# Optimization experiments

Hardware: AMD Instinct MI355X
Metric: run time of the kernel (lower is better)

## Reference

```python
import jax, jax.numpy as jnp
import numpy as np

KERNEL = 4  # conv kernel_size == stride


def setup_inputs() -> dict:
    key = jax.random.key(0)
    k1, k2, k3, k4 = jax.random.split(key, 4)
    x = jax.random.normal(k1, (16, 3, 512, 512), dtype=jnp.float32)
    w_sample = jax.random.normal(k2, (64, 3, KERNEL, KERNEL), dtype=jnp.float32) * 0.1
    b_sample = jax.random.normal(k3, (64,), dtype=jnp.float32) * 0.1
    centers = jax.random.uniform(k4, (8,), dtype=jnp.float32)
    return {"x": x, "w_sample": w_sample, "b_sample": b_sample, "centers": centers}


def _spectral_normalize(w):
    # torch spectral_norm divides the weight by its top singular value
    # (estimated by power iteration; we compute it exactly, same math at convergence)
    wm = w.reshape(w.shape[0], -1)  # [out, in*kh*kw]
    sigma = jnp.linalg.svd(wm, compute_uv=False)[0]
    return w / sigma


def _forward(x, w_sample, b_sample, centers):
    wn = _spectral_normalize(w_sample)
    # strided conv: 3 -> C channels, kernel=stride=4, no padding  -> [B,C,H/4,W/4]
    y = jax.lax.conv_general_dilated(
        x, wn, window_strides=(KERNEL, KERNEL), padding='VALID',
        dimension_numbers=('NCHW', 'OIHW', 'NCHW'))
    y = y + b_sample[None, :, None, None]
    # soft VQ: squared distance to each center, softmax(-dist)-weighted sum of centers
    quant_dist = (y[..., None] - centers) ** 2          # [B,C,H',W',K]
    soft = jnp.sum(centers * jax.nn.softmax(-quant_dist, axis=-1), axis=-1)
    return soft


def reference(x, w_sample, b_sample, centers):
    return _forward(x, w_sample, b_sample, centers)
```

## Files before the change

### kernel.cpp

```cpp
#include <hip/hip_runtime.h>
#include <stdint.h>

#define CIN 3
#define WW 512
#define HW (512 * 512)
#define COUT 64
#define KF 48
#define HO 128
#define WO 128
#define LDA 52

#define NTAB 2048
#define YMIN (-12.0f)
#define YMAX (12.0f)
#define INVH ((float)NTAB / (YMAX - YMIN))
#define WS_TAB_OFF 128
#define WS_WP 4224
#define WS_FLOATS (WS_WP + 1536)

typedef __attribute__((ext_vector_type(16))) float f32x16;
typedef __fp16 half2t __attribute__((ext_vector_type(2)));
typedef __fp16 half8 __attribute__((ext_vector_type(8)));

union H8 { half8 h; half2t h2[4]; __fp16 e[8]; uint32_t u[4]; float f[4]; };

__device__ __forceinline__ half8 cvt8_rtz(float4 a, float4 b) {
  H8 r;
  r.h2[0] = __builtin_amdgcn_cvt_pkrtz(a.x, a.y);
  r.h2[1] = __builtin_amdgcn_cvt_pkrtz(a.z, a.w);
  r.h2[2] = __builtin_amdgcn_cvt_pkrtz(b.x, b.y);
  r.h2[3] = __builtin_amdgcn_cvt_pkrtz(b.z, b.w);
  return r.h;
}

__device__ __forceinline__ float vq_eval(float y, const float* __restrict__ c) {
  float d[8], m;
#pragma unroll
  for (int k = 0; k < 8; ++k) { float t = y - c[k]; d[k] = t * t; }
  m = fminf(fminf(fminf(d[0], d[1]), fminf(d[2], d[3])),
            fminf(fminf(d[4], d[5]), fminf(d[6], d[7])));
  float num = 0.f, den = 0.f;
#pragma unroll
  for (int k = 0; k < 8; ++k) {
    float e = __expf(m - d[k]);
    den += e;
    num = fmaf(c[k], e, num);
  }
  return num / den;
}

__global__ __launch_bounds__(256) void prep_sigma(
    const float* __restrict__ w, const float* __restrict__ bias,
    const float* __restrict__ centers, float* __restrict__ ws, int build_tab) {
  const int t = threadIdx.x;

  if (blockIdx.x == 1) {
    float c[8];
#pragma unroll
    for (int k = 0; k < 8; ++k) c[k] = centers[k];
    const float h = (YMAX - YMIN) / (float)NTAB;
#pragma unroll 1
    for (int k = t; k < NTAB; k += 256) {
      float y0 = YMIN + (float)k * h;
      float f0 = vq_eval(y0, c);
      float f1 = vq_eval(y0 + h, c);
      ws[WS_TAB_OFF + 2 * k]     = f0;
      ws[WS_TAB_OFF + 2 * k + 1] = f1 - f0;
    }
    if (t < COUT) ws[2 + t] = (bias[t] - YMIN) * INVH;
    return;
  }

  __shared__ float sW[COUT * KF];
  __shared__ float sG[KF * LDA];
  __shared__ float sA[KF * LDA];
  __shared__ float sB[KF * LDA];
  __shared__ float sv[64];
  __shared__ float sp[256];
  __shared__ float s_a;

  {
    const float4* w4 = (const float4*)w;
    float4* s4 = (float4*)sW;
#pragma unroll
    for (int q = 0; q < 3; ++q) s4[q * 256 + t] = w4[q * 256 + t];
  }
  __syncthreads();

  const int ti = t >> 4, tj = t & 15;
  const int i0 = 3 * ti, j0 = 3 * tj;
  {
    float acc[3][3] = {{0.f}};
#pragma unroll 4
    for (int m = 0; m < COUT; ++m) {
      const float* wr = sW + m * KF;
      float a0 = wr[i0], a1 = wr[i0 + 1], a2 = wr[i0 + 2];
      float b0 = wr[j0], b1 = wr[j0 + 1], b2 = wr[j0 + 2];
      acc[0][0] = fmaf(a0, b0, acc[0][0]);
      acc[0][1] = fmaf(a0, b1, acc[0][1]);
      acc[0][2] = fmaf(a0, b2, acc[0][2]);
      acc[1][0] = fmaf(a1, b0, acc[1][0]);
      acc[1][1] = fmaf(a1, b1, acc[1][1]);
      acc[1][2] = fmaf(a1, b2, acc[1][2]);
      acc[2][0] = fmaf(a2, b0, acc[2][0]);
      acc[2][1] = fmaf(a2, b1, acc[2][1]);
      acc[2][2] = fmaf(a2, b2, acc[2][2]);
    }
#pragma unroll
    for (int ii = 0; ii < 3; ++ii)
#pragma unroll
      for (int jj = 0; jj < 3; ++jj) {
        sG[(i0 + ii) * LDA + j0 + jj] = acc[ii][jj];
        sA[(i0 + ii) * LDA + j0 + jj] = acc[ii][jj];
      }
  }
  __syncthreads();

#pragma unroll 1
  for (int s = 0; s < 4; ++s) {
    const float* src = (s & 1) ? sB : sA;
    float* dst = (s & 1) ? sA : sB;
    float acc[3][3] = {{0.f}};
#pragma unroll
    for (int q = 0; q < 12; ++q) {
      float4 ar0 = *(const float4*)(src + (i0 + 0) * LDA + 4 * q);
      float4 ar1 = *(const float4*)(src + (i0 + 1) * LDA + 4 * q);
      float4 ar2 = *(const float4*)(src + (i0 + 2) * LDA + 4 * q);
      float4 br0 = *(const float4*)(src + (j0 + 0) * LDA + 4 * q);
      float4 br1 = *(const float4*)(src + (j0 + 1) * LDA + 4 * q);
      float4 br2 = *(const float4*)(src + (j0 + 2) * LDA + 4 * q);
#define DOT4(A, B, C) \
      C = fmaf(A.x, B.x, C); C = fmaf(A.y, B.y, C); \
      C = fmaf(A.z, B.z, C); C = fmaf(A.w, B.w, C);
      DOT4(ar0, br0, acc[0][0]); DOT4(ar0, br1, acc[0][1]); DOT4(ar0, br2, acc[0][2]);
      DOT4(ar1, br0, acc[1][0]); DOT4(ar1, br1, acc[1][1]); DOT4(ar1, br2, acc[1][2]);
      DOT4(ar2, br0, acc[2][0]); DOT4(ar2, br1, acc[2][1]); DOT4(ar2, br2, acc[2][2]);
#undef DOT4
    }
    __syncthreads();
#pragma unroll
    for (int ii = 0; ii < 3; ++ii)
#pragma unroll
      for (int jj = 0; jj < 3; ++jj)
        dst[(i0 + ii) * LDA + j0 + jj] = acc[ii][jj];
    __syncthreads();
  }
  const float* M = sA;

  if (t < 64) sv[t] = (t < KF) ? 1.0f : 0.f;
  __syncthreads();

#pragma unroll 1
  for (int it = 0; it < 6; ++it) {
    float partial = 0.f;
    if (t < 192) {
      const int row = t >> 2, seg = t & 3;
      const float* mr = M + row * LDA + seg * 12;
      const float4* v4 = (const float4*)sv;
#pragma unroll
      for (int q = 0; q < 3; ++q) {
        float4 m4 = *(const float4*)(mr + 4 * q);
        float4 vv = v4[seg * 3 + q];
        partial = fmaf(m4.x, vv.x, partial);
        partial = fmaf(m4.y, vv.y, partial);
        partial = fmaf(m4.z, vv.z, partial);
        partial = fmaf(m4.w, vv.w, partial);
      }
    }
    sp[t] = partial;
    __syncthreads();
    if (t < 64) {
      float nv = 0.f;
      if (t < KF) nv = (sp[4 * t] + sp[4 * t + 1]) + (sp[4 * t + 2] + sp[4 * t + 3]);
      float ss = nv * nv;
#pragma unroll
      for (int m = 32; m >= 1; m >>= 1) ss += __shfl_xor(ss, m, 64);
      sv[t] = (t < KF) ? nv * rsqrtf(ss) : 0.f;
    }
    __syncthreads();
  }

  {
    float partial = 0.f;
    if (t < 192) {
      const int row = t >> 2, seg = t & 3;
      const float* mr = sG + row * LDA + seg * 12;
      const float4* v4 = (const float4*)sv;
#pragma unroll
      for (int q = 0; q < 3; ++q) {
        float4 m4 = *(const float4*)(mr + 4 * q);
        float4 vv = v4[seg * 3 + q];
        partial = fmaf(m4.x, vv.x, partial);
        partial = fmaf(m4.y, vv.y, partial);
        partial = fmaf(m4.z, vv.z, partial);
        partial = fmaf(m4.w, vv.w, partial);
      }
    }
    sp[t] = partial;
    __syncthreads();
    if (t < 64) {
      float nv = 0.f;
      if (t < KF) nv = (sp[4 * t] + sp[4 * t + 1]) + (sp[4 * t + 2] + sp[4 * t + 3]);
      float vt = sv[t];
      float num = nv * vt;
      float den = vt * vt;
#pragma unroll
      for (int m = 32; m >= 1; m >>= 1) {
        num += __shfl_xor(num, m, 64);
        den += __shfl_xor(den, m, 64);
      }
      if (t == 0) {
        float sg = sqrtf(num / den);
        ws[0] = sg;
        ws[1] = INVH / sg;
        s_a = INVH / sg;
      }
    }
  }
  __syncthreads();

  if (build_tab) {
    const float a = s_a;
#pragma unroll 1
    for (int sl = t; sl < 384; sl += 256) {
      const int grp = sl >> 6;
      const int ct = grp / 3;
      const int kk = grp % 3;
      const int l  = sl & 63;
      const int ch = ct * 32 + (l & 31);
      const int kbase = kk * 16 + (l >> 5) * 8;
      const float* src = w + ch * KF + kbase;
      float4 fa = *(const float4*)(src);
      float4 fb = *(const float4*)(src + 4);
      H8 r;
      r.e[0] = (__fp16)(fa.x * a);
      r.e[1] = (__fp16)(fa.y * a);
      r.e[2] = (__fp16)(fa.z * a);
      r.e[3] = (__fp16)(fa.w * a);
      r.e[4] = (__fp16)(fb.x * a);
      r.e[5] = (__fp16)(fb.y * a);
      r.e[6] = (__fp16)(fb.z * a);
      r.e[7] = (__fp16)(fb.w * a);
      *(float4*)(ws + WS_WP + sl * 4) =
          make_float4(r.f[0], r.f[1], r.f[2], r.f[3]);
    }
  }
}

__global__ __launch_bounds__(256) void conv_vq_mfma3(
    const float* __restrict__ x, const float* __restrict__ params,
    float* __restrict__ out) {
  __shared__ float stab[2 * NTAB];
  __shared__ float sso[COUT];
  const int t = threadIdx.x;
  {
    const float4* src = (const float4*)(params + WS_TAB_OFF);
    float4* dst = (float4*)stab;
#pragma unroll
    for (int q = 0; q < 4; ++q) dst[q * 256 + t] = src[q * 256 + t];
    if (t < COUT) sso[t] = params[2 + t];
  }
  __syncthreads();

  const int lane = t & 63;
  const int wv   = t >> 6;
  const int ct   = wv & 1;
  const int pt   = wv >> 1;
  const int h    = lane >> 5;
  const int pl   = lane & 31;

  const int n0   = blockIdx.x * 64;
  const int b    = n0 >> 14;
  const int rem0 = n0 & 16383;
  const int i    = rem0 >> 7;
  const int jj   = (rem0 & 127) + pt * 32 + pl;

  const float* xb = x + (size_t)b * (CIN * HW) + (size_t)(4 * i) * WW + 4 * jj;
  half8 Xf[3];
#pragma unroll
  for (int kk = 0; kk < 3; ++kk) {
    float4 fa = *(const float4*)(xb + (size_t)kk * HW + (2 * h) * WW);
    float4 fb = *(const float4*)(xb + (size_t)kk * HW + (2 * h + 1) * WW);
    Xf[kk] = cvt8_rtz(fa, fb);
  }

  const half8* wp = (const half8*)(params + WS_WP);
  half8 Wf[3];
#pragma unroll
  for (int kk = 0; kk < 3; ++kk) Wf[kk] = wp[(ct * 3 + kk) * 64 + lane];

  const int ch = ct * 32 + pl;
  const float och = sso[ch];
  f32x16 acc;
#pragma unroll
  for (int r = 0; r < 16; ++r) acc[r] = och;

#pragma unroll
  for (int kk = 0; kk < 3; ++kk)
    acc = __builtin_amdgcn_mfma_f32_32x32x16_f16(Xf[kk], Wf[kk], acc, 0, 0, 0);

  const float2* tab2 = (const float2*)stab;
  float* ob = out + ((size_t)(b * COUT + ch)) * 16384 + i * 128 +
              (rem0 & 127) + pt * 32 + 4 * h;
#pragma unroll
  for (int q = 0; q < 4; ++q) {
    float4 res;
#pragma unroll
    for (int m = 0; m < 4; ++m) {
      float u = acc[4 * q + m];
      u = fmaxf(u, 0.0f);
      u = fminf(u, (float)NTAB - 0.0005f);
      const int k = (int)u;
      const float fr = u - (float)k;
      const float2 e = tab2[k];
      float v = fmaf(fr, e.y, e.x);
      if (m == 0) res.x = v; else if (m == 1) res.y = v;
      else if (m == 2) res.z = v; else res.w = v;
    }
    *(float4*)(ob + 8 * q) = res;
  }
}

__global__ __launch_bounds__(256) void conv_vq_exp(
    const float* __restrict__ x, const float* __restrict__ w,
    const float* __restrict__ bias, const float* __restrict__ centers,
    const float* __restrict__ sigma_ptr, float* __restrict__ out) {
  const int t = threadIdx.x;
  const int pos = blockIdx.x * 256 + t;
  const int b   = pos >> 14;
  const int rem = pos & 16383;
  const int i   = rem >> 7;
  const int j   = rem & 127;

  const float inv_sigma = 1.0f / sigma_ptr[0];
  float cc[8], tc[8], mc2[8];
#pragma unroll
  for (int k = 0; k < 8; ++k) {
    float c = centers[k];
    cc[k] = c; tc[k] = 2.0f * c; mc2[k] = -c * c;
  }
  const float* xp = x + (size_t)b * (CIN * HW) + (size_t)(4 * i) * WW + 4 * j;
  float p[KF];
#pragma unroll
  for (int ci = 0; ci < CIN; ++ci)
#pragma unroll
    for (int kh = 0; kh < 4; ++kh) {
      float4 v4 = *(const float4*)(xp + (size_t)ci * HW + kh * WW);
      p[(ci * 4 + kh) * 4 + 0] = v4.x;
      p[(ci * 4 + kh) * 4 + 1] = v4.y;
      p[(ci * 4 + kh) * 4 + 2] = v4.z;
      p[(ci * 4 + kh) * 4 + 3] = v4.w;
    }
  float* op = out + (size_t)b * (COUT * HO * WO) + rem;
#pragma unroll 2
  for (int c = 0; c < COUT; ++c) {
    const float4* wr = (const float4*)(w + c * KF);
    float a0 = 0.f, a1 = 0.f, a2 = 0.f, a3 = 0.f;
#pragma unroll
    for (int q = 0; q < 12; ++q) {
      float4 gq = wr[q];
      a0 = fmaf(p[4*q+0], gq.x, a0);
      a1 = fmaf(p[4*q+1], gq.y, a1);
      a2 = fmaf(p[4*q+2], gq.z, a2);
      a3 = fmaf(p[4*q+3], gq.w, a3);
    }
    const float y = fmaf((a0 + a1) + (a2 + a3), inv_sigma, bias[c]);
    float e0 = __expf(fmaf(tc[0], y, mc2[0])), e1 = __expf(fmaf(tc[1], y, mc2[1]));
    float e2 = __expf(fmaf(tc[2], y, mc2[2])), e3 = __expf(fmaf(tc[3], y, mc2[3]));
    float e4 = __expf(fmaf(tc[4], y, mc2[4])), e5 = __expf(fmaf(tc[5], y, mc2[5]));
    float e6 = __expf(fmaf(tc[6], y, mc2[6])), e7 = __expf(fmaf(tc[7], y, mc2[7]));
    float den = ((e0 + e1) + (e2 + e3)) + ((e4 + e5) + (e6 + e7));
    float num = (fmaf(cc[0], e0, cc[1] * e1) + fmaf(cc[2], e2, cc[3] * e3)) +
                (fmaf(cc[4], e4, cc[5] * e5) + fmaf(cc[6], e6, cc[7] * e7));
    op[(size_t)c * (HO * WO)] = __fdividef(num, den);
  }
}

extern "C" void kernel_launch(void* const* d_in, const int* in_sizes, int n_in,
                              void* d_out, int out_size, void* d_ws, size_t ws_size,
                              hipStream_t stream) {
  const float* x       = (const float*)d_in[0];
  const float* w       = (const float*)d_in[1];
  const float* b       = (const float*)d_in[2];
  const float* centers = (const float*)d_in[3];
  float* out = (float*)d_out;
  float* ws  = (float*)d_ws;

  const int use_table = (ws_size >= (size_t)WS_FLOATS * sizeof(float)) ? 1 : 0;

  prep_sigma<<<use_table ? 2 : 1, 256, 0, stream>>>(w, b, centers, ws, use_table);
  if (use_table)
    conv_vq_mfma3<<<(16 * HO * WO) / 64, 256, 0, stream>>>(x, ws, out);
  else
    conv_vq_exp<<<(16 * HO * WO) / 256, 256, 0, stream>>>(x, w, b, centers, ws, out);
}
```

Baseline: 41.15 us.

## Process two tiles per block, shrink VQ lookup table, use nontemporal stores

```diff
diff --git a/kernel.cpp b/kernel.cpp
--- a/kernel.cpp
+++ b/kernel.cpp
@@ -10,15 +10,16 @@
 #define WO 128
 #define LDA 52
 
-#define NTAB 2048
+#define NTAB 512
 #define YMIN (-12.0f)
 #define YMAX (12.0f)
 #define INVH ((float)NTAB / (YMAX - YMIN))
 #define WS_TAB_OFF 128
-#define WS_WP 4224
+#define WS_WP (WS_TAB_OFF + 2 * NTAB)
 #define WS_FLOATS (WS_WP + 1536)
 
 typedef __attribute__((ext_vector_type(16))) float f32x16;
+typedef __attribute__((ext_vector_type(4))) float f32x4v;
 typedef __fp16 half2t __attribute__((ext_vector_type(2)));
 typedef __fp16 half8 __attribute__((ext_vector_type(8)));
 
@@ -247,7 +248,7 @@
   }
 }
 
-__global__ __launch_bounds__(256) void conv_vq_mfma3(
+__global__ __launch_bounds__(256) void conv_vq_mfma4(
     const float* __restrict__ x, const float* __restrict__ params,
     float* __restrict__ out) {
   __shared__ float stab[2 * NTAB];
@@ -255,9 +256,7 @@
   const int t = threadIdx.x;
   {
     const float4* src = (const float4*)(params + WS_TAB_OFF);
-    float4* dst = (float4*)stab;
-#pragma unroll
-    for (int q = 0; q < 4; ++q) dst[q * 256 + t] = src[q * 256 + t];
+    ((float4*)stab)[t] = src[t];
     if (t < COUT) sso[t] = params[2 + t];
   }
   __syncthreads();
@@ -269,20 +268,9 @@
   const int h    = lane >> 5;
   const int pl   = lane & 31;
 
-  const int n0   = blockIdx.x * 64;
+  const int n0   = blockIdx.x * 128;
   const int b    = n0 >> 14;
-  const int rem0 = n0 & 16383;
-  const int i    = rem0 >> 7;
-  const int jj   = (rem0 & 127) + pt * 32 + pl;
-
-  const float* xb = x + (size_t)b * (CIN * HW) + (size_t)(4 * i) * WW + 4 * jj;
-  half8 Xf[3];
-#pragma unroll
-  for (int kk = 0; kk < 3; ++kk) {
-    float4 fa = *(const float4*)(xb + (size_t)kk * HW + (2 * h) * WW);
-    float4 fb = *(const float4*)(xb + (size_t)kk * HW + (2 * h + 1) * WW);
-    Xf[kk] = cvt8_rtz(fa, fb);
-  }
+  const int i    = (n0 & 16383) >> 7;
 
   const half8* wp = (const half8*)(params + WS_WP);
   half8 Wf[3];
@@ -291,33 +279,47 @@
 
   const int ch = ct * 32 + pl;
   const float och = sso[ch];
-  f32x16 acc;
-#pragma unroll
-  for (int r = 0; r < 16; ++r) acc[r] = och;
-
-#pragma unroll
-  for (int kk = 0; kk < 3; ++kk)
-    acc = __builtin_amdgcn_mfma_f32_32x32x16_f16(Xf[kk], Wf[kk], acc, 0, 0, 0);
-
+  const float* xrow = x + (size_t)b * (CIN * HW) + (size_t)(4 * i) * WW;
   const float2* tab2 = (const float2*)stab;
-  float* ob = out + ((size_t)(b * COUT + ch)) * 16384 + i * 128 +
-              (rem0 & 127) + pt * 32 + 4 * h;
-#pragma unroll
-  for (int q = 0; q < 4; ++q) {
-    float4 res;
-#pragma unroll
-    for (int m = 0; m < 4; ++m) {
-      float u = acc[4 * q + m];
-      u = fmaxf(u, 0.0f);
-      u = fminf(u, (float)NTAB - 0.0005f);
-      const int k = (int)u;
-      const float fr = u - (float)k;
-      const float2 e = tab2[k];
-      float v = fmaf(fr, e.y, e.x);
-      if (m == 0) res.x = v; else if (m == 1) res.y = v;
-      else if (m == 2) res.z = v; else res.w = v;
-    }
-    *(float4*)(ob + 8 * q) = res;
+  float* obase = out + ((size_t)(b * COUT + ch)) * 16384 + i * 128;
+
+#pragma unroll
+  for (int it = 0; it < 2; ++it) {
+    const int jj = it * 64 + pt * 32 + pl;
+
+    const float* xb = xrow + 4 * jj;
+    half8 Xf[3];
+#pragma unroll
+    for (int kk = 0; kk < 3; ++kk) {
+      float4 fa = *(const float4*)(xb + (size_t)kk * HW + (2 * h) * WW);
+      float4 fb = *(const float4*)(xb + (size_t)kk * HW + (2 * h + 1) * WW);
+      Xf[kk] = cvt8_rtz(fa, fb);
+    }
+
+    f32x16 acc;
+#pragma unroll
+    for (int r = 0; r < 16; ++r) acc[r] = och;
+
+#pragma unroll
+    for (int kk = 0; kk < 3; ++kk)
+      acc = __builtin_amdgcn_mfma_f32_32x32x16_f16(Xf[kk], Wf[kk], acc, 0, 0, 0);
+
+    float* ob = obase + it * 64 + pt * 32 + 4 * h;
+#pragma unroll
+    for (int q = 0; q < 4; ++q) {
+      f32x4v res;
+#pragma unroll
+      for (int m = 0; m < 4; ++m) {
+        float u = acc[4 * q + m];
+        u = fmaxf(u, 0.0f);
+        u = fminf(u, (float)NTAB - 0.0005f);
+        const int k = (int)u;
+        const float fr = u - (float)k;
+        const float2 e = tab2[k];
+        res[m] = fmaf(fr, e.y, e.x);
+      }
+      __builtin_nontemporal_store(res, (f32x4v*)(ob + 8 * q));
+    }
   }
 }
 
@@ -390,7 +392,7 @@
 
   prep_sigma<<<use_table ? 2 : 1, 256, 0, stream>>>(w, b, centers, ws, use_table);
   if (use_table)
-    conv_vq_mfma3<<<(16 * HO * WO) / 64, 256, 0, stream>>>(x, ws, out);
+    conv_vq_mfma4<<<(16 * HO * WO) / 128, 256, 0, stream>>>(x, ws, out);
   else
     conv_vq_exp<<<(16 * HO * WO) / 256, 256, 0, stream>>>(x, w, b, centers, ws, out);
 }
```

Result: slower. 78.33 us (+90.4%).
